# Kernel optimization log

Hardware: AMD Instinct MI355X
Metric: run time of the kernel (lower is better)

## Reference

```python
import jax, jax.numpy as jnp
import numpy as np

V, D, H, L, T, B, F = 32000, 768, 12, 6, 2048, 1, 3072
EPS = 1e-5


def _ln(x, g, b):
    m = jnp.mean(x, axis=-1, keepdims=True)
    v = jnp.mean((x - m) ** 2, axis=-1, keepdims=True)
    return (x - m) / jnp.sqrt(v + EPS) * g + b


def setup_inputs() -> dict:
    key = jax.random.key(0)
    ks = jax.random.split(key, 12)
    s = 0.02  # init std per _init_weights
    tok_emb = jax.random.normal(ks[0], (V, D), jnp.float32) * s
    tok_emb = tok_emb.at[0].set(0.0)  # padding_idx=0 row zeroed
    pos_emb = jax.random.normal(ks[1], (T, D), jnp.float32) * s
    Wqkv = jax.random.normal(ks[2], (L, 3 * D, D), jnp.float32) * s
    Wo = jax.random.normal(ks[3], (L, D, D), jnp.float32) * s
    W1 = jax.random.normal(ks[4], (L, F, D), jnp.float32) * s
    b1 = jnp.zeros((L, F), jnp.float32)
    W2 = jax.random.normal(ks[5], (L, D, F), jnp.float32) * s
    b2 = jnp.zeros((L, D), jnp.float32)
    ln1_g = jnp.ones((L, D), jnp.float32); ln1_b = jnp.zeros((L, D), jnp.float32)
    ln2_g = jnp.ones((L, D), jnp.float32); ln2_b = jnp.zeros((L, D), jnp.float32)
    lnf_g = jnp.ones((D,), jnp.float32); lnf_b = jnp.zeros((D,), jnp.float32)
    x = jax.random.randint(ks[6], (B, T), 0, V, jnp.int32)
    targets = jax.random.randint(ks[7], (B, T), 0, V, jnp.int32)
    return dict(x=x, targets=targets, tok_emb=tok_emb, pos_emb=pos_emb,
                Wqkv=Wqkv, Wo=Wo, ln1_g=ln1_g, ln1_b=ln1_b, ln2_g=ln2_g,
                ln2_b=ln2_b, W1=W1, b1=b1, W2=W2, b2=b2, lnf_g=lnf_g, lnf_b=lnf_b)


def reference(x, targets, tok_emb, pos_emb, Wqkv, Wo, ln1_g, ln1_b,
              ln2_g, ln2_b, W1, b1, W2, b2, lnf_g, lnf_b):
    Bv, Tv = x.shape
    dh = D // H
    h = tok_emb[x] + pos_emb[:Tv][None]  # [B,T,D]
    causal = jnp.tril(jnp.ones((Tv, Tv), bool))
    for l in range(L):
        # --- attention sublayer (pre-LN) ---
        hn = _ln(h, ln1_g[l], ln1_b[l])
        qkv = hn @ Wqkv[l].T  # [B,T,3D]
        q, k, v = jnp.split(qkv, 3, axis=-1)
        q = q.reshape(Bv, Tv, H, dh).transpose(0, 2, 1, 3)
        k = k.reshape(Bv, Tv, H, dh).transpose(0, 2, 1, 3)
        v = v.reshape(Bv, Tv, H, dh).transpose(0, 2, 1, 3)
        scores = jnp.einsum('bhqd,bhkd->bhqk', q, k) / (dh ** 0.5)
        scores = jnp.where(causal, scores, -jnp.inf)
        attn = jax.nn.softmax(scores, axis=-1)
        ctx = jnp.einsum('bhqk,bhkd->bhqd', attn, v)
        ctx = ctx.transpose(0, 2, 1, 3).reshape(Bv, Tv, D)
        h = h + ctx @ Wo[l].T
        # --- FFN sublayer (pre-LN) ---
        hn = _ln(h, ln2_g[l], ln2_b[l])
        ff = jax.nn.gelu(hn @ W1[l].T + b1[l], approximate=False) @ W2[l].T + b2[l]
        h = h + ff
    h = _ln(h, lnf_g, lnf_b)
    logits = h @ tok_emb.T  # tied output head [B,T,V]
    # cross_entropy with ignore_index=0 (mean over non-ignored)
    logp = jax.nn.log_softmax(logits, axis=-1)
    nll = -jnp.take_along_axis(logp, targets[..., None], axis=-1)[..., 0]
    valid = (targets != 0).astype(logits.dtype)
    loss = jnp.sum(nll * valid) / jnp.maximum(jnp.sum(valid), 1.0)
    return (logits, loss)
```

## Files before the change

### kernel.cpp

```cpp
#include <hip/hip_runtime.h>


typedef unsigned short ushort_t;
typedef unsigned int uint_t;
typedef __bf16 bf16x8 __attribute__((ext_vector_type(8)));
typedef float floatx4 __attribute__((ext_vector_type(4)));

#define D_ 768
#define T_ 2048
#define H_ 12
#define L_ 6
#define F_ 3072
#define V_ 32000

__device__ __forceinline__ float b2f(ushort_t u) {
    union { uint_t i; float f; } v; v.i = ((uint_t)u) << 16; return v.f;
}
__device__ __forceinline__ ushort_t f2b(float f) {
    uint_t x = __builtin_bit_cast(uint_t, f);
    uint_t r = (x + 0x7fffu + ((x >> 16) & 1u)) >> 16;
    return (ushort_t)r;
}
__device__ __forceinline__ float ldf(const void* p, size_t idx, int isbf) {
    return isbf ? b2f(((const ushort_t*)p)[idx]) : ((const float*)p)[idx];
}
__device__ __forceinline__ float wave_sum(float v) {
    for (int o = 32; o; o >>= 1) v += __shfl_xor(v, o);
    return v;
}
__device__ __forceinline__ float wave_max(float v) {
    for (int o = 32; o; o >>= 1) v = fmaxf(v, __shfl_xor(v, o));
    return v;
}

__global__ void sniff_kernel(const void* __restrict__ pos, int* __restrict__ flag) {
    if (threadIdx.x == 0 && blockIdx.x == 0) {
        const uint_t* w = (const uint_t*)pos;
        int c = 0;
        for (int i = 0; i < 64; ++i) {
            uint_t lo = w[i] & 0xffffu;
            int e = (int)((lo >> 7) & 0xff);
            if (e >= 110 && e < 127) ++c;
        }
        *flag = (c >= 32) ? 1 : 0;
    }
}

__global__ __launch_bounds__(256) void embed_kernel(
    const int* __restrict__ x, const void* __restrict__ tok,
    const void* __restrict__ pos, float* __restrict__ h,
    const int* __restrict__ flagp) {
    const int isbf = *flagp;
    int t = blockIdx.x, tid = threadIdx.x;
    int id = x[t];
    float* hr = h + (size_t)t * D_;
#pragma unroll
    for (int e = 0; e < 3; ++e) {
        int d = tid + e * 256;
        hr[d] = ldf(tok, (size_t)id * D_ + d, isbf) +
                ldf(pos, (size_t)t * D_ + d, isbf);
    }
}

__global__ __launch_bounds__(256) void ln_kernel(
    const float* __restrict__ x, const void* __restrict__ g, size_t go,
    const void* __restrict__ b, size_t bo, ushort_t* __restrict__ out,
    const int* __restrict__ flagp) {
    const int isbf = *flagp;
    int row = blockIdx.x, tid = threadIdx.x;
    int lane = tid & 63, wid = tid >> 6;
    const float* xr = x + (size_t)row * D_;
    float v0 = xr[tid], v1 = xr[tid + 256], v2 = xr[tid + 512];
    __shared__ float s1[4], s2[4];
    float s = wave_sum(v0 + v1 + v2);
    if (!lane) s1[wid] = s;
    __syncthreads();
    float mean = (s1[0] + s1[1] + s1[2] + s1[3]) * (1.f / 768.f);
    float d0 = v0 - mean, d1 = v1 - mean, d2 = v2 - mean;
    float q = wave_sum(d0 * d0 + d1 * d1 + d2 * d2);
    if (!lane) s2[wid] = q;
    __syncthreads();
    float var = (s2[0] + s2[1] + s2[2] + s2[3]) * (1.f / 768.f);
    float rstd = rsqrtf(var + 1e-5f);
    ushort_t* orow = out + (size_t)row * D_;
    orow[tid] = f2b(d0 * rstd * ldf(g, go + tid, isbf) + ldf(b, bo + tid, isbf));
    orow[tid + 256] = f2b(d1 * rstd * ldf(g, go + tid + 256, isbf) + ldf(b, bo + tid + 256, isbf));
    orow[tid + 512] = f2b(d2 * rstd * ldf(g, go + tid + 512, isbf) + ldf(b, bo + tid + 512, isbf));
}

template <int EPI>
__global__ __launch_bounds__(256) void gemm_bt(
    const ushort_t* __restrict__ A, const void* __restrict__ B, size_t Bo,
    const void* __restrict__ bias, size_t biaso, ushort_t* __restrict__ obf,
    float* __restrict__ resid, int M, int N, int K,
    const int* __restrict__ flagp) {
    const int isbf = *flagp;
    __shared__ ushort_t lds[8192];
    const int tid = threadIdx.x;
    const int lane = tid & 63;
    const int wid = tid >> 6;
    const int wm = wid >> 1, wn = wid & 1;
    const int m0 = (EPI == 4 ? (int)blockIdx.x : (int)blockIdx.y) * 128;
    const int n0 = (EPI == 4 ? (int)blockIdx.y : (int)blockIdx.x) * 128;
    const int lm = lane & 15, lq = lane >> 4;

    floatx4 acc[4][4] = {};

    const int arow = tid >> 2, aseg = tid & 3;
    const int sidx = (((arow * 64) + (aseg << 4)) ^ ((arow & 7) << 4)) >> 1;
    const ushort_t* gA = A + (size_t)(m0 + arow) * K + aseg * 8;
    const size_t bofs = Bo + (size_t)(n0 + arow) * K + aseg * 8;
    const ushort_t* gBh = (const ushort_t*)B + bofs;
    const float* gBf = (const float*)B + bofs;
    ushort_t* sA = lds;
    ushort_t* sB = lds + 4096;

    for (int k0 = 0; k0 < K; k0 += 32) {
        *(uint4*)(sA + sidx) = *(const uint4*)(gA + k0);
        *(uint4*)(sA + 2048 + sidx) = *(const uint4*)(gA + (size_t)64 * K + k0);
        if (isbf) {
            *(uint4*)(sB + sidx) = *(const uint4*)(gBh + k0);
            *(uint4*)(sB + 2048 + sidx) = *(const uint4*)(gBh + (size_t)64 * K + k0);
        } else {
            union { ushort_t u[8]; uint4 v; } p0, p1;
            float4 x0 = *(const float4*)(gBf + k0);
            float4 x1 = *(const float4*)(gBf + k0 + 4);
            float4 y0 = *(const float4*)(gBf + (size_t)64 * K + k0);
            float4 y1 = *(const float4*)(gBf + (size_t)64 * K + k0 + 4);
            p0.u[0] = f2b(x0.x); p0.u[1] = f2b(x0.y); p0.u[2] = f2b(x0.z); p0.u[3] = f2b(x0.w);
            p0.u[4] = f2b(x1.x); p0.u[5] = f2b(x1.y); p0.u[6] = f2b(x1.z); p0.u[7] = f2b(x1.w);
            p1.u[0] = f2b(y0.x); p1.u[1] = f2b(y0.y); p1.u[2] = f2b(y0.z); p1.u[3] = f2b(y0.w);
            p1.u[4] = f2b(y1.x); p1.u[5] = f2b(y1.y); p1.u[6] = f2b(y1.z); p1.u[7] = f2b(y1.w);
            *(uint4*)(sB + sidx) = p0.v;
            *(uint4*)(sB + 2048 + sidx) = p1.v;
        }
        __syncthreads();
        bf16x8 af[4], bfr[4];
#pragma unroll
        for (int f = 0; f < 4; ++f) {
            const int ar = wm * 64 + f * 16 + lm;
            const int br = wn * 64 + f * 16 + lm;
            af[f] = *(const bf16x8*)(sA + ((((ar * 64) + (lq << 4)) ^ ((ar & 7) << 4)) >> 1));
            bfr[f] = *(const bf16x8*)(sB + ((((br * 64) + (lq << 4)) ^ ((br & 7) << 4)) >> 1));
        }
#pragma unroll
        for (int i = 0; i < 4; ++i)
#pragma unroll
            for (int j = 0; j < 4; ++j)
                acc[i][j] = __builtin_amdgcn_mfma_f32_16x16x32_bf16(
                    af[i], bfr[j], acc[i][j], 0, 0, 0);
        __syncthreads();
    }

#pragma unroll
    for (int i = 0; i < 4; ++i) {
#pragma unroll
        for (int j = 0; j < 4; ++j) {
#pragma unroll
            for (int r = 0; r < 4; ++r) {
                int row = m0 + wm * 64 + i * 16 + lq * 4 + r;
                int col = n0 + wn * 64 + j * 16 + lm;
                float c = acc[i][j][r];
                if (EPI == 1 || EPI == 3) c += ldf(bias, biaso + col, isbf);
                if (EPI == 1) c = 0.5f * c * (1.f + erff(c * 0.70710678118f));
                size_t idx = (size_t)row * N + col;
                if (EPI == 0 || EPI == 1) {
                    obf[idx] = f2b(c);
                } else if (EPI == 4) {
                    if (isbf) obf[idx] = f2b(c);
                    else ((float*)obf)[idx] = c;
                } else {
                    resid[idx] += c;
                }
            }
        }
    }
}

__global__ __launch_bounds__(256) void attn_mfma(
    const ushort_t* __restrict__ qkv, ushort_t* __restrict__ ctx) {
    __shared__ __attribute__((aligned(16))) ushort_t sK[64 * 72];
    __shared__ __attribute__((aligned(16))) ushort_t sVT[64 * 72];
    __shared__ __attribute__((aligned(16))) ushort_t sP[64 * 72];

    const int tid = threadIdx.x;
    const int lane = tid & 63;
    const int w = tid >> 6;
    const int lm = lane & 15, lq = lane >> 4;
    const int qt = (int)gridDim.x - 1 - (int)blockIdx.x;
    const int q0 = qt * 64;
    const int h = blockIdx.y;

    bf16x8 qf[2];
    {
        const int qrow = q0 + w * 16 + lm;
        const ushort_t* src = qkv + (size_t)qrow * (3 * D_) + h * 64 + lq * 8;
#pragma unroll
        for (int kk = 0; kk < 2; ++kk) {
            union { ushort_t u[8]; uint4 v; bf16x8 b; } tmp;
            tmp.v = *(const uint4*)(src + kk * 32);
#pragma unroll
            for (int e = 0; e < 8; ++e) tmp.u[e] = f2b(b2f(tmp.u[e]) * 0.125f);
            qf[kk] = tmp.b;
        }
    }

    floatx4 acc_o[4] = {};
    float m[4], l[4];
#pragma unroll
    for (int r = 0; r < 4; ++r) { m[r] = -1e30f; l[r] = 0.f; }

    const int krow_s = tid >> 3;
    const int seg = tid & 7;
    ushort_t* pw = sP + w * (16 * 72);

    for (int j0 = 0; j0 <= q0; j0 += 64) {
#pragma unroll
        for (int p = 0; p < 2; ++p) {
            const int kr = p * 32 + krow_s;
            const size_t rb = (size_t)(j0 + kr) * (3 * D_) + h * 64 + seg * 8;
            *(uint4*)(sK + kr * 72 + seg * 8) = *(const uint4*)(qkv + rb + D_);
            union { ushort_t u[8]; uint4 v; } tv;
            tv.v = *(const uint4*)(qkv + rb + 2 * D_);
#pragma unroll
            for (int e = 0; e < 8; ++e) sVT[(seg * 8 + e) * 72 + kr] = tv.u[e];
        }
        __syncthreads();

        floatx4 sa[4] = {};
#pragma unroll
        for (int nf = 0; nf < 4; ++nf) {
#pragma unroll
            for (int kk = 0; kk < 2; ++kk) {
                bf16x8 kf = *(const bf16x8*)(sK + (nf * 16 + lm) * 72 + kk * 32 + lq * 8);
                sa[nf] = __builtin_amdgcn_mfma_f32_16x16x32_bf16(qf[kk], kf, sa[nf], 0, 0, 0);
            }
        }
        if (j0 == q0) {
#pragma unroll
            for (int nf = 0; nf < 4; ++nf)
#pragma unroll
                for (int r = 0; r < 4; ++r)
                    if (j0 + nf * 16 + lm > q0 + w * 16 + lq * 4 + r) sa[nf][r] = -1e30f;
        }

        float rmax[4];
#pragma unroll
        for (int r = 0; r < 4; ++r)
            rmax[r] = fmaxf(fmaxf(sa[0][r], sa[1][r]), fmaxf(sa[2][r], sa[3][r]));
#pragma unroll
        for (int r = 0; r < 4; ++r) {
            rmax[r] = fmaxf(rmax[r], __shfl_xor(rmax[r], 1));
            rmax[r] = fmaxf(rmax[r], __shfl_xor(rmax[r], 2));
            rmax[r] = fmaxf(rmax[r], __shfl_xor(rmax[r], 4));
            rmax[r] = fmaxf(rmax[r], __shfl_xor(rmax[r], 8));
        }
        float alpha[4], rsum[4];
#pragma unroll
        for (int r = 0; r < 4; ++r) {
            float mn = fmaxf(m[r], rmax[r]);
            alpha[r] = __expf(m[r] - mn);
            m[r] = mn;
            rsum[r] = 0.f;
        }
#pragma unroll
        for (int nf = 0; nf < 4; ++nf)
#pragma unroll
            for (int r = 0; r < 4; ++r) {
                float pe = __expf(sa[nf][r] - m[r]);
                rsum[r] += pe;
                pw[(lq * 4 + r) * 72 + nf * 16 + lm] = f2b(pe);
            }
#pragma unroll
        for (int r = 0; r < 4; ++r) {
            rsum[r] += __shfl_xor(rsum[r], 1);
            rsum[r] += __shfl_xor(rsum[r], 2);
            rsum[r] += __shfl_xor(rsum[r], 4);
            rsum[r] += __shfl_xor(rsum[r], 8);
            l[r] = l[r] * alpha[r] + rsum[r];
        }
#pragma unroll
        for (int nf = 0; nf < 4; ++nf)
#pragma unroll
            for (int r = 0; r < 4; ++r) acc_o[nf][r] *= alpha[r];

        bf16x8 pa[2];
#pragma unroll
        for (int kk = 0; kk < 2; ++kk)
            pa[kk] = *(const bf16x8*)(pw + lm * 72 + kk * 32 + lq * 8);
#pragma unroll
        for (int nf = 0; nf < 4; ++nf) {
#pragma unroll
            for (int kk = 0; kk < 2; ++kk) {
                bf16x8 vf = *(const bf16x8*)(sVT + (nf * 16 + lm) * 72 + kk * 32 + lq * 8);
                acc_o[nf] = __builtin_amdgcn_mfma_f32_16x16x32_bf16(pa[kk], vf, acc_o[nf], 0, 0, 0);
            }
        }
        __syncthreads();
    }

    float inv[4];
#pragma unroll
    for (int r = 0; r < 4; ++r) inv[r] = 1.f / fmaxf(l[r], 1e-30f);
#pragma unroll
    for (int nf = 0; nf < 4; ++nf)
#pragma unroll
        for (int r = 0; r < 4; ++r) {
            int q = q0 + w * 16 + lq * 4 + r;
            ctx[(size_t)q * D_ + h * 64 + nf * 16 + lm] = f2b(acc_o[nf][r] * inv[r]);
        }
}

__global__ __launch_bounds__(256) void loss_rows(
    const void* __restrict__ logits, const int* __restrict__ tg,
    float* __restrict__ rowacc, const int* __restrict__ flagp) {
    const int isbf = *flagp;
    int t = blockIdx.x, tid = threadIdx.x;
    int lane = tid & 63, wid = tid >> 6;
    const ushort_t* lrh = (const ushort_t*)logits + (size_t)t * V_;
    const float* lrf = (const float*)logits + (size_t)t * V_;
    __shared__ float sm[4], ss[4];
    float mx = -1e30f;
    for (int j = tid; j < V_ / 8; j += 256) {
        float v[8];
        if (isbf) {
            uint4 u = ((const uint4*)lrh)[j];
            uint_t w[4] = {u.x, u.y, u.z, u.w};
#pragma unroll
            for (int p = 0; p < 4; ++p) {
                v[p * 2] = b2f((ushort_t)(w[p] & 0xffff));
                v[p * 2 + 1] = b2f((ushort_t)(w[p] >> 16));
            }
        } else {
            float4 a = ((const float4*)lrf)[j * 2];
            float4 bq = ((const float4*)lrf)[j * 2 + 1];
            v[0] = a.x; v[1] = a.y; v[2] = a.z; v[3] = a.w;
            v[4] = bq.x; v[5] = bq.y; v[6] = bq.z; v[7] = bq.w;
        }
#pragma unroll
        for (int p = 0; p < 8; ++p) mx = fmaxf(mx, v[p]);
    }
    mx = wave_max(mx);
    if (!lane) sm[wid] = mx;
    __syncthreads();
    mx = fmaxf(fmaxf(sm[0], sm[1]), fmaxf(sm[2], sm[3]));
    float se = 0.f;
    for (int j = tid; j < V_ / 8; j += 256) {
        float v[8];
        if (isbf) {
            uint4 u = ((const uint4*)lrh)[j];
            uint_t w[4] = {u.x, u.y, u.z, u.w};
#pragma unroll
            for (int p = 0; p < 4; ++p) {
                v[p * 2] = b2f((ushort_t)(w[p] & 0xffff));
                v[p * 2 + 1] = b2f((ushort_t)(w[p] >> 16));
            }
        } else {
            float4 a = ((const float4*)lrf)[j * 2];
            float4 bq = ((const float4*)lrf)[j * 2 + 1];
            v[0] = a.x; v[1] = a.y; v[2] = a.z; v[3] = a.w;
            v[4] = bq.x; v[5] = bq.y; v[6] = bq.z; v[7] = bq.w;
        }
#pragma unroll
        for (int p = 0; p < 8; ++p) se += __expf(v[p] - mx);
    }
    se = wave_sum(se);
    if (!lane) ss[wid] = se;
    __syncthreads();
    if (tid == 0) {
        se = ss[0] + ss[1] + ss[2] + ss[3];
        int tv = tg[t];
        float lv = isbf ? b2f(lrh[tv]) : lrf[tv];
        float nll = mx + __logf(se) - lv;
        rowacc[t] = (tv != 0) ? nll : 0.f;
        rowacc[T_ + t] = (tv != 0) ? 1.f : 0.f;
    }
}

__global__ __launch_bounds__(256) void loss_final(
    const float* __restrict__ rowacc, void* __restrict__ out,
    const int* __restrict__ flagp) {
    const int isbf = *flagp;
    int tid = threadIdx.x;
    int lane = tid & 63, wid = tid >> 6;
    float s = 0.f, c = 0.f;
    for (int i = tid; i < T_; i += 256) { s += rowacc[i]; c += rowacc[T_ + i]; }
    __shared__ float sa[4], sb[4];
    s = wave_sum(s); c = wave_sum(c);
    if (!lane) { sa[wid] = s; sb[wid] = c; }
    __syncthreads();
    if (tid == 0) {
        float S = sa[0] + sa[1] + sa[2] + sa[3];
        float C = sb[0] + sb[1] + sb[2] + sb[3];
        float loss = S / fmaxf(C, 1.f);
        size_t o = (size_t)T_ * V_;
        if (isbf) ((ushort_t*)out)[o] = f2b(loss);
        else ((float*)out)[o] = loss;
    }
}

extern "C" void kernel_launch(void* const* d_in, const int* in_sizes, int n_in,
                              void* d_out, int out_size, void* d_ws,
                              size_t ws_size, hipStream_t stream) {
    const int* x = (const int*)d_in[0];
    const int* targets = (const int*)d_in[1];
    const void* tok_emb = d_in[2];
    const void* pos_emb = d_in[3];
    const void* Wqkv = d_in[4];
    const void* Wo = d_in[5];
    const void* ln1_g = d_in[6];
    const void* ln1_b = d_in[7];
    const void* ln2_g = d_in[8];
    const void* ln2_b = d_in[9];
    const void* W1 = d_in[10];
    const void* b1 = d_in[11];
    const void* W2 = d_in[12];
    const void* b2 = d_in[13];
    const void* lnf_g = d_in[14];
    const void* lnf_b = d_in[15];

    char* ws = (char*)d_ws;
    float* h = (float*)ws;
    ushort_t* hn = (ushort_t*)(ws + 6291456);
    ushort_t* qkvb = (ushort_t*)(ws + 9437184);
    ushort_t* ctxb = (ushort_t*)(ws + 18874368);
    ushort_t* ff1 = qkvb;
    float* rowacc = (float*)(ws + 22020096);
    int* d_flag = (int*)(ws + 22036480);

    sniff_kernel<<<1, 64, 0, stream>>>(pos_emb, d_flag);
    embed_kernel<<<T_, 256, 0, stream>>>(x, tok_emb, pos_emb, h, d_flag);

    for (int l = 0; l < L_; ++l) {
        size_t oln = (size_t)l * D_;
        ln_kernel<<<T_, 256, 0, stream>>>(h, ln1_g, oln, ln1_b, oln, hn, d_flag);
        gemm_bt<0><<<dim3(3 * D_ / 128, T_ / 128), 256, 0, stream>>>(
            hn, Wqkv, (size_t)l * 3 * D_ * D_, nullptr, 0, qkvb, nullptr,
            T_, 3 * D_, D_, d_flag);
        attn_mfma<<<dim3(T_ / 64, H_), 256, 0, stream>>>(qkvb, ctxb);
        gemm_bt<2><<<dim3(D_ / 128, T_ / 128), 256, 0, stream>>>(
            ctxb, Wo, (size_t)l * D_ * D_, nullptr, 0, nullptr, h,
            T_, D_, D_, d_flag);
        ln_kernel<<<T_, 256, 0, stream>>>(h, ln2_g, oln, ln2_b, oln, hn, d_flag);
        gemm_bt<1><<<dim3(F_ / 128, T_ / 128), 256, 0, stream>>>(
            hn, W1, (size_t)l * F_ * D_, b1, (size_t)l * F_, ff1, nullptr,
            T_, F_, D_, d_flag);
        gemm_bt<3><<<dim3(D_ / 128, T_ / 128), 256, 0, stream>>>(
            ff1, W2, (size_t)l * D_ * F_, b2, (size_t)l * D_, nullptr, h,
            T_, D_, F_, d_flag);
    }

    ln_kernel<<<T_, 256, 0, stream>>>(h, lnf_g, 0, lnf_b, 0, hn, d_flag);
    gemm_bt<4><<<dim3(T_ / 128, V_ / 128), 256, 0, stream>>>(
        hn, tok_emb, 0, nullptr, 0, (ushort_t*)d_out, nullptr,
        T_, V_, D_, d_flag);
    loss_rows<<<T_, 256, 0, stream>>>(d_out, targets, rowacc, d_flag);
    loss_final<<<1, 256, 0, stream>>>(rowacc, d_out, d_flag);
}
```

Before: 2.865 ms.

## Double-buffer attention K/V tiles, swizzle logits GEMM blocks, single-pass online loss

The attention kernel now prefetches the next K/V tile into registers while computing the current one. It commits that tile to a second LDS buffer and stores V transposed in packed pairs with an XOR swizzle to reduce bank conflicts. The logits GEMM (EPI 4) remaps block IDs so that consecutive blocks share N tiles within an XCD, aiming for better L2 reuse of the embedding matrix. The loss kernel fuses its max and sum-exp passes into one online-softmax pass, so each logits row is read once instead of twice. The changes add register pressure and hardcoded grid-shape constants in exchange.

Result: faster. 2.756 ms (-3.8%).

```diff
diff --git a/kernel.cpp b/kernel.cpp
--- a/kernel.cpp
+++ b/kernel.cpp
@@ -100,8 +100,23 @@
     const int lane = tid & 63;
     const int wid = tid >> 6;
     const int wm = wid >> 1, wn = wid & 1;
-    const int m0 = (EPI == 4 ? (int)blockIdx.x : (int)blockIdx.y) * 128;
-    const int n0 = (EPI == 4 ? (int)blockIdx.y : (int)blockIdx.x) * 128;
+    int m0, n0;
+    if (EPI == 4) {
+        int bid = (int)blockIdx.x + 16 * (int)blockIdx.y;
+        int mblk, nblk;
+        if (bid < 3968) {
+            int xcd = bid & 7, j = bid >> 3;
+            mblk = j & 15;
+            nblk = xcd + 8 * (j >> 4);
+        } else {
+            int u = bid - 3968;
+            nblk = 248 + (u >> 4);
+            mblk = u & 15;
+        }
+        m0 = mblk * 128; n0 = nblk * 128;
+    } else {
+        m0 = (int)blockIdx.y * 128; n0 = (int)blockIdx.x * 128;
+    }
     const int lm = lane & 15, lq = lane >> 4;
 
     floatx4 acc[4][4] = {};
@@ -179,9 +194,9 @@
 
 __global__ __launch_bounds__(256) void attn_mfma(
     const ushort_t* __restrict__ qkv, ushort_t* __restrict__ ctx) {
-    __shared__ __attribute__((aligned(16))) ushort_t sK[64 * 72];
-    __shared__ __attribute__((aligned(16))) ushort_t sVT[64 * 72];
-    __shared__ __attribute__((aligned(16))) ushort_t sP[64 * 72];
+    __shared__ __attribute__((aligned(16))) ushort_t sK[2][64 * 72];
+    __shared__ __attribute__((aligned(16))) ushort_t sVT[2][64 * 80];
+    __shared__ __attribute__((aligned(16))) ushort_t sP[4][16 * 72];
 
     const int tid = threadIdx.x;
     const int lane = tid & 63;
@@ -210,38 +225,58 @@
 #pragma unroll
     for (int r = 0; r < 4; ++r) { m[r] = -1e30f; l[r] = 0.f; }
 
-    const int krow_s = tid >> 3;
+    const int k2 = tid >> 3;
     const int seg = tid & 7;
-    ushort_t* pw = sP + w * (16 * 72);
-
-    for (int j0 = 0; j0 <= q0; j0 += 64) {
-#pragma unroll
-        for (int p = 0; p < 2; ++p) {
-            const int kr = p * 32 + krow_s;
-            const size_t rb = (size_t)(j0 + kr) * (3 * D_) + h * 64 + seg * 8;
-            *(uint4*)(sK + kr * 72 + seg * 8) = *(const uint4*)(qkv + rb + D_);
-            union { ushort_t u[8]; uint4 v; } tv;
-            tv.v = *(const uint4*)(qkv + rb + 2 * D_);
-#pragma unroll
-            for (int e = 0; e < 8; ++e) sVT[(seg * 8 + e) * 72 + kr] = tv.u[e];
-        }
-        __syncthreads();
+    const size_t colo = (size_t)h * 64 + seg * 8;
+    const int vslot = 2 * (k2 ^ (seg << 2));
+    ushort_t* pw = sP[w];
+
+    uint4 kreg[2], vreg[2];
+    auto issue = [&](int j0) {
+        const ushort_t* r0 = qkv + (size_t)(j0 + 2 * k2) * (3 * D_) + colo;
+        kreg[0] = *(const uint4*)(r0 + D_);
+        vreg[0] = *(const uint4*)(r0 + 2 * D_);
+        const ushort_t* r1 = r0 + 3 * D_;
+        kreg[1] = *(const uint4*)(r1 + D_);
+        vreg[1] = *(const uint4*)(r1 + 2 * D_);
+    };
+    auto commit = [&](int b) {
+        *(uint4*)(&sK[b][(2 * k2) * 72 + seg * 8]) = kreg[0];
+        *(uint4*)(&sK[b][(2 * k2 + 1) * 72 + seg * 8]) = kreg[1];
+        union { uint4 v; ushort_t u[8]; } v0, v1;
+        v0.v = vreg[0]; v1.v = vreg[1];
+#pragma unroll
+        for (int e = 0; e < 8; ++e) {
+            const int d = seg * 8 + e;
+            *(uint_t*)(&sVT[b][d * 80 + vslot]) =
+                (uint_t)v0.u[e] | ((uint_t)v1.u[e] << 16);
+        }
+    };
+
+    const int nt = qt;
+    issue(0);
+    commit(0);
+    __syncthreads();
+
+    for (int t = 0; t <= nt; ++t) {
+        const int cur = t & 1;
+        if (t < nt) issue((t + 1) * 64);
 
         floatx4 sa[4] = {};
 #pragma unroll
         for (int nf = 0; nf < 4; ++nf) {
 #pragma unroll
             for (int kk = 0; kk < 2; ++kk) {
-                bf16x8 kf = *(const bf16x8*)(sK + (nf * 16 + lm) * 72 + kk * 32 + lq * 8);
+                bf16x8 kf = *(const bf16x8*)(&sK[cur][(nf * 16 + lm) * 72 + kk * 32 + lq * 8]);
                 sa[nf] = __builtin_amdgcn_mfma_f32_16x16x32_bf16(qf[kk], kf, sa[nf], 0, 0, 0);
             }
         }
-        if (j0 == q0) {
+        if (t == nt) {
 #pragma unroll
             for (int nf = 0; nf < 4; ++nf)
 #pragma unroll
                 for (int r = 0; r < 4; ++r)
-                    if (j0 + nf * 16 + lm > q0 + w * 16 + lq * 4 + r) sa[nf][r] = -1e30f;
+                    if (nf * 16 + lm > w * 16 + lq * 4 + r) sa[nf][r] = -1e30f;
         }
 
         float rmax[4];
@@ -287,15 +322,19 @@
         bf16x8 pa[2];
 #pragma unroll
         for (int kk = 0; kk < 2; ++kk)
-            pa[kk] = *(const bf16x8*)(pw + lm * 72 + kk * 32 + lq * 8);
+            pa[kk] = *(const bf16x8*)(&pw[lm * 72 + kk * 32 + lq * 8]);
 #pragma unroll
         for (int nf = 0; nf < 4; ++nf) {
+            const int d = nf * 16 + lm;
 #pragma unroll
             for (int kk = 0; kk < 2; ++kk) {
-                bf16x8 vf = *(const bf16x8*)(sVT + (nf * 16 + lm) * 72 + kk * 32 + lq * 8);
+                const int p0 = (kk * 16 + lq * 4) ^ (((d >> 3) & 7) << 2);
+                bf16x8 vf = *(const bf16x8*)(&sVT[cur][d * 80 + 2 * p0]);
                 acc_o[nf] = __builtin_amdgcn_mfma_f32_16x16x32_bf16(pa[kk], vf, acc_o[nf], 0, 0, 0);
             }
         }
+
+        if (t < nt) commit(cur ^ 1);
         __syncthreads();
     }
 
@@ -320,7 +359,7 @@
     const ushort_t* lrh = (const ushort_t*)logits + (size_t)t * V_;
     const float* lrf = (const float*)logits + (size_t)t * V_;
     __shared__ float sm[4], ss[4];
-    float mx = -1e30f;
+    float mx = -1e30f, se = 0.f;
     for (int j = tid; j < V_ / 8; j += 256) {
         float v[8];
         if (isbf) {
@@ -337,41 +376,25 @@
             v[0] = a.x; v[1] = a.y; v[2] = a.z; v[3] = a.w;
             v[4] = bq.x; v[5] = bq.y; v[6] = bq.z; v[7] = bq.w;
         }
-#pragma unroll
-        for (int p = 0; p < 8; ++p) mx = fmaxf(mx, v[p]);
-    }
-    mx = wave_max(mx);
-    if (!lane) sm[wid] = mx;
-    __syncthreads();
-    mx = fmaxf(fmaxf(sm[0], sm[1]), fmaxf(sm[2], sm[3]));
-    float se = 0.f;
-    for (int j = tid; j < V_ / 8; j += 256) {
-        float v[8];
-        if (isbf) {
-            uint4 u = ((const uint4*)lrh)[j];
-            uint_t w[4] = {u.x, u.y, u.z, u.w};
-#pragma unroll
-            for (int p = 0; p < 4; ++p) {
-                v[p * 2] = b2f((ushort_t)(w[p] & 0xffff));
-                v[p * 2 + 1] = b2f((ushort_t)(w[p] >> 16));
-            }
-        } else {
-            float4 a = ((const float4*)lrf)[j * 2];
-            float4 bq = ((const float4*)lrf)[j * 2 + 1];
-            v[0] = a.x; v[1] = a.y; v[2] = a.z; v[3] = a.w;
-            v[4] = bq.x; v[5] = bq.y; v[6] = bq.z; v[7] = bq.w;
-        }
-#pragma unroll
-        for (int p = 0; p < 8; ++p) se += __expf(v[p] - mx);
-    }
-    se = wave_sum(se);
-    if (!lane) ss[wid] = se;
+        float m8 = fmaxf(fmaxf(fmaxf(v[0], v[1]), fmaxf(v[2], v[3])),
+                         fmaxf(fmaxf(v[4], v[5]), fmaxf(v[6], v[7])));
+        float nm = fmaxf(mx, m8);
+        se *= __expf(mx - nm);
+#pragma unroll
+        for (int p = 0; p < 8; ++p) se += __expf(v[p] - nm);
+        mx = nm;
+    }
+    float M = wave_max(mx);
+    se = wave_sum(se * __expf(mx - M));
+    if (!lane) { sm[wid] = M; ss[wid] = se; }
     __syncthreads();
     if (tid == 0) {
-        se = ss[0] + ss[1] + ss[2] + ss[3];
+        float bm = fmaxf(fmaxf(sm[0], sm[1]), fmaxf(sm[2], sm[3]));
+        float bs = ss[0] * __expf(sm[0] - bm) + ss[1] * __expf(sm[1] - bm) +
+                   ss[2] * __expf(sm[2] - bm) + ss[3] * __expf(sm[3] - bm);
         int tv = tg[t];
         float lv = isbf ? b2f(lrh[tv]) : lrf[tv];
-        float nll = mx + __logf(se) - lv;
+        float nll = bm + __logf(bs) - lv;
         rowacc[t] = (tv != 0) ? nll : 0.f;
         rowacc[T_ + t] = (tv != 0) ? 1.f : 0.f;
     }
```
